# Kernel tuning notes

Measured on AMD Instinct MI355X. Metric: run time of the kernel, lower is better.

The kernel has to match this reference:

```python
import jax, jax.numpy as jnp
import numpy as np

N = 50000      # nodes
E = 800000     # edges (before self loops)
IN = 128       # in_channels
HID = 128      # 2*out_channels
OUT = 64       # out_channels
NEG_SLOPE = 0.2


def _gat_conv(x, src, dst, W, a_src, a_dst, b, n_nodes):
    """Single-head PyG GATConv (concat=True, heads=1, self-loops already added)."""
    h = x @ W                                   # [N, F]
    alpha_s = h @ a_src                         # [N]
    alpha_d = h @ a_dst                         # [N]
    e = alpha_s[src] + alpha_d[dst]             # [E'] logits per edge j->i
    e = jnp.where(e > 0, e, NEG_SLOPE * e)      # LeakyReLU(0.2)
    # segment softmax over destination node
    m = jax.ops.segment_max(e, dst, num_segments=n_nodes)   # [N]
    w = jnp.exp(e - m[dst])                                   # [E']
    denom = jax.ops.segment_sum(w, dst, num_segments=n_nodes) # [N]
    alpha = w / denom[dst]                                     # [E']
    out = jax.ops.segment_sum(alpha[:, None] * h[src], dst, num_segments=n_nodes)
    return out + b


def _with_self_loops(edge_index, n_nodes):
    loop = jnp.arange(n_nodes, dtype=edge_index.dtype)
    src = jnp.concatenate([edge_index[0], loop])
    dst = jnp.concatenate([edge_index[1], loop])
    return src, dst


def setup_inputs() -> dict:
    key = jax.random.key(0)
    ks = jax.random.split(key, 10)
    s = 0.1
    return {
        "x": jax.random.normal(ks[0], (N, IN), jnp.float32),
        "edge_index": jax.random.randint(ks[1], (2, E), 0, N, jnp.int32),
        "W1": jax.random.normal(ks[2], (IN, HID), jnp.float32) * s,
        "a1_src": jax.random.normal(ks[3], (HID,), jnp.float32) * s,
        "a1_dst": jax.random.normal(ks[4], (HID,), jnp.float32) * s,
        "b1": jnp.zeros((HID,), jnp.float32),
        "W2": jax.random.normal(ks[5], (HID, OUT), jnp.float32) * s,
        "a2_src": jax.random.normal(ks[6], (OUT,), jnp.float32) * s,
        "a2_dst": jax.random.normal(ks[7], (OUT,), jnp.float32) * s,
        "b2": jnp.zeros((OUT,), jnp.float32),
    }


def reference(x, edge_index, W1, a1_src, a1_dst, b1, W2, a2_src, a2_dst, b2):
    src, dst = _with_self_loops(edge_index, N)
    h = _gat_conv(x, src, dst, W1, a1_src, a1_dst, b1, N)
    h = jax.nn.relu(h)
    return _gat_conv(h, src, dst, W2, a2_src, a2_dst, b2, N)
```

## Files before the change

kernel.cpp:

```cpp
#include <hip/hip_runtime.h>
#include <hip/hip_bf16.h>


#define BCAP 4096

typedef __attribute__((ext_vector_type(8))) short bf16x8;
typedef __attribute__((ext_vector_type(4))) float f32x4;

__device__ __forceinline__ unsigned short bf16bits(float f){
  __hip_bfloat16 b = __float2bfloat16(f);
  return *(unsigned short*)&b;
}
__device__ __forceinline__ float bf16lo(unsigned int v){ return __uint_as_float(v << 16); }
__device__ __forceinline__ float bf16hi(unsigned int v){ return __uint_as_float(v & 0xFFFF0000u); }

__global__ __launch_bounds__(256) void prep_w_both(
    const float* __restrict__ W1, const float* __restrict__ W2,
    const float* __restrict__ a2s, const float* __restrict__ a2d,
    unsigned short* __restrict__ W1t, unsigned short* __restrict__ W2t,
    float* __restrict__ vas, float* __restrict__ vad)
{
  int b = blockIdx.x, t = threadIdx.x;
  if (b < 48){
    int idx = b*256 + t;
    if (idx < 8192){
      int n = idx >> 6, k2 = idx & 63;
      float a = W1[(size_t)(2*k2)*128 + n];
      float c = W1[(size_t)(2*k2+1)*128 + n];
      ushort2 o; o.x = bf16bits(a); o.y = bf16bits(c);
      *(ushort2*)&W1t[(size_t)n*128 + 2*k2] = o;
    } else {
      int r = idx - 8192;
      int n = r >> 6, k2 = r & 63;
      float a = W2[(size_t)(2*k2)*64 + n];
      float c = W2[(size_t)(2*k2+1)*64 + n];
      ushort2 o; o.x = bf16bits(a); o.y = bf16bits(c);
      *(ushort2*)&W2t[(size_t)n*128 + 2*k2] = o;
    }
  } else {
    int k = t & 127;
    const float* av = (t < 128) ? a2s : a2d;
    float* ov = (t < 128) ? vas : vad;
    float s = 0.f;
    for (int n=0; n<64; n++) s += W2[(size_t)k*64 + n] * av[n];
    ov[k] = s;
  }
}

template<int NC, bool FUSE>
__device__ __forceinline__ void gemm_body(
    const float* __restrict__ Af, const unsigned short* __restrict__ Ah,
    const unsigned short* __restrict__ Wt,
    const float* __restrict__ avs, const float* __restrict__ avd,
    unsigned short* __restrict__ H, float* __restrict__ as_, float* __restrict__ ad_,
    int M, int rowBase, unsigned short* As, unsigned short* Ws)
{
  const int K = 128;
  int t = threadIdx.x;
  if (Af){
    #pragma unroll
    for (int i=0;i<8;i++){
      int idx = t + i*256; int r = idx>>5, k4 = idx&31;
      int grow = rowBase + r;
      float4 v = (grow<M) ? *(const float4*)&Af[(size_t)grow*K + k4*4]
                          : make_float4(0.f,0.f,0.f,0.f);
      ushort4 o; o.x=bf16bits(v.x); o.y=bf16bits(v.y); o.z=bf16bits(v.z); o.w=bf16bits(v.w);
      *(ushort4*)&As[r*136 + k4*4] = o;
    }
  } else {
    #pragma unroll
    for (int i=0;i<4;i++){
      int idx = t + i*256; int r = idx>>4, k8 = idx&15;
      int grow = rowBase + r;
      uint4 v = (grow<M) ? *(const uint4*)&Ah[(size_t)grow*K + k8*8]
                         : make_uint4(0u,0u,0u,0u);
      *(uint4*)&As[r*136 + k8*8] = v;
    }
  }
  #pragma unroll
  for (int i=0;i<NC/16;i++){
    int idx = t + i*256; int n = idx>>4, k8 = idx&15;
    *(uint4*)&Ws[n*136 + k8*8] = *(const uint4*)&Wt[(size_t)n*K + k8*8];
  }
  __syncthreads();

  int wave = t>>6, lane = t&63, ln = lane&15, q = lane>>4;
  f32x4 acc[NC/16];
  #pragma unroll
  for (int nt=0; nt<NC/16; nt++) acc[nt] = (f32x4){0.f,0.f,0.f,0.f};
  #pragma unroll
  for (int kk=0;kk<4;kk++){
    bf16x8 a = *(const bf16x8*)&As[(wave*16+ln)*136 + kk*32 + q*8];
    #pragma unroll
    for (int nt=0; nt<NC/16; nt++){
      bf16x8 b = *(const bf16x8*)&Ws[(nt*16+ln)*136 + kk*32 + q*8];
      acc[nt] = __builtin_amdgcn_mfma_f32_16x16x32_bf16(a, b, acc[nt], 0, 0, 0);
    }
  }
  float asl[NC/16], adl[NC/16];
  if (FUSE){
    #pragma unroll
    for (int nt=0; nt<NC/16; nt++){ asl[nt]=avs[nt*16+ln]; adl[nt]=avd[nt*16+ln]; }
  }
  #pragma unroll
  for (int i=0;i<4;i++){
    int grow = rowBase + wave*16 + q*4 + i;
    if (grow < M){
      float ps=0.f, pd=0.f;
      #pragma unroll
      for (int nt=0; nt<NC/16; nt++){
        float v = acc[nt][i];
        H[(size_t)grow*NC + nt*16 + ln] = bf16bits(v);
        if (FUSE){ ps += v*asl[nt]; pd += v*adl[nt]; }
      }
      if (FUSE){
        #pragma unroll
        for (int d=1; d<16; d<<=1){ ps += __shfl_xor(ps,d); pd += __shfl_xor(pd,d); }
        if (ln==0){ atomicAdd(&as_[grow], ps); atomicAdd(&ad_[grow], pd); }
      }
    }
  }
}

__global__ __launch_bounds__(256) void scatter_or_gemm(
    const int* __restrict__ src, const int* __restrict__ dst,
    int* __restrict__ bucketCount, unsigned int* __restrict__ gbuf, int E, int B,
    const float* __restrict__ x, const unsigned short* __restrict__ W1t,
    const float* __restrict__ a1s, const float* __restrict__ a1d,
    unsigned short* __restrict__ h1, float* __restrict__ as1, float* __restrict__ ad1,
    int M)
{
  __shared__ unsigned short smem[64*136 + 128*136];
  int t = threadIdx.x;
  if ((int)blockIdx.x >= B){
    gemm_body<128, true>(x, nullptr, W1t, a1s, a1d, h1, as1, ad1, M,
                         (blockIdx.x - B)*64, smem, smem + 64*136);
    return;
  }
  int* hist = (int*)smem;
  int* base = hist + 512;
  int e0 = blockIdx.x * 2048;
  hist[t] = 0; hist[t+256] = 0;
  __syncthreads();
  int sv[8], dv[8];
  #pragma unroll
  for (int k=0;k<8;k++){
    int i = e0 + t + k*256;
    if (i < E){ sv[k]=src[i]; dv[k]=dst[i]; atomicAdd(&hist[dv[k]>>7], 1); }
    else { sv[k] = -1; dv[k] = 0; }
  }
  __syncthreads();
  int h0 = hist[t], h1c = hist[t+256];
  if (h0 > 0)  base[t]     = atomicAdd(&bucketCount[t],     h0);
  if (h1c > 0) base[t+256] = atomicAdd(&bucketCount[t+256], h1c);
  __syncthreads();
  hist[t] = 0; hist[t+256] = 0;
  __syncthreads();
  #pragma unroll
  for (int k=0;k<8;k++){
    if (sv[k] >= 0){
      int b = dv[k] >> 7;
      int r = base[b] + atomicAdd(&hist[b], 1);
      if (r < BCAP)
        gbuf[(size_t)b*BCAP + r] = ((unsigned)(dv[k] & 127) << 16) | (unsigned)sv[k];
    }
  }
}

__global__ __launch_bounds__(256) void fine_sort(
    const unsigned int* __restrict__ gbuf, const int* __restrict__ bucketCount,
    int* __restrict__ offs, int* __restrict__ srcS, int N, int E, int B)
{
  __shared__ int sh[512];
  __shared__ int h[128];
  __shared__ int pre[128];
  __shared__ int rank[128];
  int b = blockIdx.x, t = threadIdx.x;
  {
    int i0 = t, i1 = t + 256;
    int nd0 = 0, nd1 = 0;
    if (i0 < B){ int lo=i0*128; nd0 = (N-lo<128)?(N-lo):128; }
    if (i1 < B){ int lo=i1*128; nd1 = (N-lo<128)?(N-lo):128; }
    sh[i0] = (i0 < B ? bucketCount[i0] : 0) + nd0;
    sh[i1] = (i1 < B ? bucketCount[i1] : 0) + nd1;
    __syncthreads();
    for (int d=1; d<512; d<<=1){
      int x0 = (i0 >= d) ? sh[i0-d] : 0;
      int x1 = (i1 >= d) ? sh[i1-d] : 0;
      __syncthreads();
      sh[i0] += x0; sh[i1] += x1;
      __syncthreads();
    }
  }
  int cnt = bucketCount[b]; if (cnt > BCAP) cnt = BCAP;
  int lo = b*128;
  int nd = (N - lo < 128) ? (N - lo) : 128;
  int base = sh[b] - (cnt + nd);
  if (b == 0 && t == 0) offs[N] = E + N;
  if (t < 128){ h[t] = 0; rank[t] = 0; }
  __syncthreads();
  for (int i = t; i < cnt; i += 256)
    atomicAdd(&h[(gbuf[(size_t)b*BCAP + i] >> 16) & 127], 1);
  __syncthreads();
  if (t < 128) pre[t] = (t < nd) ? (h[t] + 1) : 0;
  __syncthreads();
  for (int d=1; d<128; d<<=1){
    int x = (t >= d && t < 128) ? pre[t-d] : 0;
    __syncthreads();
    if (t < 128) pre[t] += x;
    __syncthreads();
  }
  int seg = (t < nd) ? (h[t] + 1) : 0;
  int ex  = (t < 128) ? (pre[t] - seg) : 0;
  if (t < nd){
    offs[lo + t] = base + ex;
    srcS[base + ex] = lo + t;
  }
  __syncthreads();
  if (t < 128) pre[t] = ex;
  __syncthreads();
  for (int i = t; i < cnt; i += 256){
    unsigned e = gbuf[(size_t)b*BCAP + i];
    int dl = (e >> 16) & 127;
    int s  = e & 0xFFFF;
    int r  = atomicAdd(&rank[dl], 1);
    srcS[base + pre[dl] + 1 + r] = s;
  }
}

__global__ __launch_bounds__(256) void edge_agg128(
    const int* __restrict__ offs, const int* __restrict__ srcS,
    const float* __restrict__ asrc, const float* __restrict__ adst,
    const unsigned short* __restrict__ Hin, const float* __restrict__ bias,
    unsigned short* __restrict__ outp,
    const float* __restrict__ vas, const float* __restrict__ vad,
    float* __restrict__ as2, float* __restrict__ ad2, int n)
{
  int wid  = (blockIdx.x * 256 + threadIdx.x) >> 6;
  int lane = threadIdx.x & 63;
  if (wid >= n) return;
  int beg = offs[wid], end = offs[wid+1];
  float ad = adst[wid];
  int qw = lane >> 4, ql = lane & 15;
  float acc[8] = {}; float denom = 0.f;
  for (int base = beg; base < end; base += 64){
    int m = end - base; if (m > 64) m = 64;
    int   sv = (lane < m) ? srcS[base + lane] : 0;
    float av = (lane < m) ? asrc[sv] : 0.f;
    float ev = av + ad;
    ev = (ev > 0.f) ? ev : 0.2f*ev;
    float wv = (lane < m) ? __expf(ev) : 0.f;
    for (int j = 0; j < m; j += 4){
      int idx = j + qw;
      int   s = __shfl(sv, idx);
      float w = __shfl(wv, idx);
      uint4 hv = *(const uint4*)&Hin[(size_t)s*128 + ql*8];
      denom += w;
      acc[0]+=w*bf16lo(hv.x); acc[1]+=w*bf16hi(hv.x);
      acc[2]+=w*bf16lo(hv.y); acc[3]+=w*bf16hi(hv.y);
      acc[4]+=w*bf16lo(hv.z); acc[5]+=w*bf16hi(hv.z);
      acc[6]+=w*bf16lo(hv.w); acc[7]+=w*bf16hi(hv.w);
    }
  }
  denom += __shfl_xor(denom,16); denom += __shfl_xor(denom,32);
  #pragma unroll
  for (int k=0;k<8;k++){ acc[k]+=__shfl_xor(acc[k],16); acc[k]+=__shfl_xor(acc[k],32); }
  if (qw == 0){
    float inv = 1.0f / denom;
    float ps = 0.f, pd = 0.f;
    unsigned short o[8];
    #pragma unroll
    for (int k=0;k<8;k++){
      float v = fmaxf(acc[k]*inv + bias[ql*8+k], 0.f);
      o[k] = bf16bits(v);
      ps += v * vas[ql*8+k];
      pd += v * vad[ql*8+k];
    }
    *(uint4*)&outp[(size_t)wid*128 + ql*8] = *(uint4*)o;
    #pragma unroll
    for (int d=1; d<16; d<<=1){ ps += __shfl_xor(ps,d); pd += __shfl_xor(pd,d); }
    if (ql == 0){ as2[wid] = ps; ad2[wid] = pd; }
  }
}

__global__ __launch_bounds__(256) void gemm2_k(
    const unsigned short* __restrict__ A, const unsigned short* __restrict__ Wt,
    unsigned short* __restrict__ H, int M)
{
  __shared__ unsigned short smem[64*136 + 64*136];
  gemm_body<64, false>(nullptr, A, Wt, nullptr, nullptr, H, nullptr, nullptr,
                       M, blockIdx.x*64, smem, smem + 64*136);
}

__global__ __launch_bounds__(256) void edge_agg64(
    const int* __restrict__ offs, const int* __restrict__ srcS,
    const float* __restrict__ asrc, const float* __restrict__ adst,
    const unsigned short* __restrict__ Hin, const float* __restrict__ bias,
    float* __restrict__ outp, int n)
{
  int wid  = (blockIdx.x * 256 + threadIdx.x) >> 6;
  int lane = threadIdx.x & 63;
  if (wid >= n) return;
  int beg = offs[wid], end = offs[wid+1];
  float ad = adst[wid];
  int ew = lane >> 3, el = lane & 7;
  float acc[8] = {}; float denom = 0.f;
  for (int base = beg; base < end; base += 64){
    int m = end - base; if (m > 64) m = 64;
    int   sv = (lane < m) ? srcS[base + lane] : 0;
    float av = (lane < m) ? asrc[sv] : 0.f;
    float ev = av + ad;
    ev = (ev > 0.f) ? ev : 0.2f*ev;
    float wv = (lane < m) ? __expf(ev) : 0.f;
    for (int j = 0; j < m; j += 8){
      int idx = j + ew;
      int   s = __shfl(sv, idx);
      float w = __shfl(wv, idx);
      uint4 hv = *(const uint4*)&Hin[(size_t)s*64 + el*8];
      denom += w;
      acc[0]+=w*bf16lo(hv.x); acc[1]+=w*bf16hi(hv.x);
      acc[2]+=w*bf16lo(hv.y); acc[3]+=w*bf16hi(hv.y);
      acc[4]+=w*bf16lo(hv.z); acc[5]+=w*bf16hi(hv.z);
      acc[6]+=w*bf16lo(hv.w); acc[7]+=w*bf16hi(hv.w);
    }
  }
  denom += __shfl_xor(denom,8); denom += __shfl_xor(denom,16); denom += __shfl_xor(denom,32);
  #pragma unroll
  for (int k=0;k<8;k++){
    acc[k]+=__shfl_xor(acc[k],8); acc[k]+=__shfl_xor(acc[k],16); acc[k]+=__shfl_xor(acc[k],32);
  }
  if (ew == 0){
    float inv = 1.0f / denom;
    float4 o0, o1;
    o0.x = acc[0]*inv + bias[el*8+0]; o0.y = acc[1]*inv + bias[el*8+1];
    o0.z = acc[2]*inv + bias[el*8+2]; o0.w = acc[3]*inv + bias[el*8+3];
    o1.x = acc[4]*inv + bias[el*8+4]; o1.y = acc[5]*inv + bias[el*8+5];
    o1.z = acc[6]*inv + bias[el*8+6]; o1.w = acc[7]*inv + bias[el*8+7];
    *(float4*)&outp[(size_t)wid*64 + el*8]     = o0;
    *(float4*)&outp[(size_t)wid*64 + el*8 + 4] = o1;
  }
}

extern "C" void kernel_launch(void* const* d_in, const int* in_sizes, int n_in,
                              void* d_out, int out_size, void* d_ws, size_t ws_size,
                              hipStream_t stream) {
  const int IN = 128, HID = 128, OUT = 64;
  const int N = in_sizes[0] / IN;
  const int E = in_sizes[1] / 2;
  const int B = (N + 127) / 128;

  const float* x    = (const float*)d_in[0];
  const int*   ei   = (const int*)d_in[1];
  const float* W1   = (const float*)d_in[2];
  const float* a1s  = (const float*)d_in[3];
  const float* a1d  = (const float*)d_in[4];
  const float* b1   = (const float*)d_in[5];
  const float* W2   = (const float*)d_in[6];
  const float* a2s  = (const float*)d_in[7];
  const float* a2d  = (const float*)d_in[8];
  const float* b2   = (const float*)d_in[9];
  float* out = (float*)d_out;

  char* w = (char*)d_ws;
  unsigned short* W1t = (unsigned short*)w; w += (size_t)HID*IN*2;
  unsigned short* W2t = (unsigned short*)w; w += (size_t)OUT*HID*2;
  unsigned short* h1    = (unsigned short*)w; w += (size_t)N*128*2;
  unsigned short* hrelu = (unsigned short*)w; w += (size_t)N*128*2;
  unsigned short* h2 = h1;
  float* as1   = (float*)w; w += (size_t)N*4;
  float* ad1   = (float*)w; w += (size_t)N*4;
  float* as2   = (float*)w; w += (size_t)N*4;
  float* ad2   = (float*)w; w += (size_t)N*4;
  float* vas   = (float*)w; w += 128*4;
  float* vad   = (float*)w; w += 128*4;
  int* offs    = (int*)w;   w += (size_t)(N+1)*4;
  int* bucketCount = (int*)w; w += 512*4;
  int* srcS    = (int*)w;   w += (size_t)(E+N)*4;
  unsigned int* gbuf = (unsigned int*)w; w += (size_t)B*BCAP*4;

  const int* esrc = ei;
  const int* edst = ei + E;

  hipMemsetAsync(bucketCount, 0, 512*4, stream);
  hipMemsetAsync(as1, 0, (size_t)2*N*4, stream);
  hipLaunchKernelGGL(prep_w_both, dim3(49), dim3(256), 0, stream,
                     W1, W2, a2s, a2d, W1t, W2t, vas, vad);
  hipLaunchKernelGGL(scatter_or_gemm, dim3(B + (N+63)/64), dim3(256), 0, stream,
                     esrc, edst, bucketCount, gbuf, E, B,
                     x, W1t, a1s, a1d, h1, as1, ad1, N);
  hipLaunchKernelGGL(fine_sort, dim3(B), dim3(256), 0, stream,
                     gbuf, bucketCount, offs, srcS, N, E, B);
  hipLaunchKernelGGL(edge_agg128, dim3((N*64+255)/256), dim3(256), 0, stream,
                     offs, srcS, as1, ad1, h1, b1, hrelu, vas, vad, as2, ad2, N);
  hipLaunchKernelGGL(gemm2_k, dim3((N+63)/64), dim3(256), 0, stream,
                     hrelu, W2t, h2, N);
  hipLaunchKernelGGL(edge_agg64, dim3((N*64+255)/256), dim3(256), 0, stream,
                     offs, srcS, as2, ad2, h2, b2, out, N);
}
```

Measured before the change: 210.9 us.

## Fold memsets into prep kernel, chunk W staging, widen fine_sort, unroll gathers

Replaces the two hipMemsetAsync calls with extra blocks in the prep kernel that zero bucketCount and the attention-score buffers, removing two launches. The layer-1 GEMM now stages W in two 64-column chunks, halving its shared memory so more blocks can be resident, at the cost of an extra barrier pair. fine_sort runs with 512 threads per block and a simpler one-element-per-thread scan. Both edge aggregation loops now process two neighbours per iteration so that more gather loads are in flight.

```diff
diff --git a/kernel.cpp b/kernel.cpp
--- a/kernel.cpp
+++ b/kernel.cpp
@@ -14,11 +14,12 @@
 __device__ __forceinline__ float bf16lo(unsigned int v){ return __uint_as_float(v << 16); }
 __device__ __forceinline__ float bf16hi(unsigned int v){ return __uint_as_float(v & 0xFFFF0000u); }
 
-__global__ __launch_bounds__(256) void prep_w_both(
+__global__ __launch_bounds__(256) void prep_all(
     const float* __restrict__ W1, const float* __restrict__ W2,
     const float* __restrict__ a2s, const float* __restrict__ a2d,
     unsigned short* __restrict__ W1t, unsigned short* __restrict__ W2t,
-    float* __restrict__ vas, float* __restrict__ vad)
+    float* __restrict__ vas, float* __restrict__ vad,
+    float* __restrict__ zeroBase, int nZero4, int* __restrict__ bucketCount)
 {
   int b = blockIdx.x, t = threadIdx.x;
   if (b < 48){
@@ -37,13 +38,19 @@
       ushort2 o; o.x = bf16bits(a); o.y = bf16bits(c);
       *(ushort2*)&W2t[(size_t)n*128 + 2*k2] = o;
     }
-  } else {
+  } else if (b == 48){
     int k = t & 127;
     const float* av = (t < 128) ? a2s : a2d;
     float* ov = (t < 128) ? vas : vad;
     float s = 0.f;
     for (int n=0; n<64; n++) s += W2[(size_t)k*64 + n] * av[n];
     ov[k] = s;
+  } else if (b == 49){
+    bucketCount[t] = 0; bucketCount[t+256] = 0;
+  } else {
+    int idx4 = (b-50)*256 + t;
+    if (idx4 < nZero4)
+      ((float4*)zeroBase)[idx4] = make_float4(0.f,0.f,0.f,0.f);
   }
 }
 
@@ -77,24 +84,28 @@
       *(uint4*)&As[r*136 + k8*8] = v;
     }
   }
-  #pragma unroll
-  for (int i=0;i<NC/16;i++){
-    int idx = t + i*256; int n = idx>>4, k8 = idx&15;
-    *(uint4*)&Ws[n*136 + k8*8] = *(const uint4*)&Wt[(size_t)n*K + k8*8];
-  }
-  __syncthreads();
-
   int wave = t>>6, lane = t&63, ln = lane&15, q = lane>>4;
   f32x4 acc[NC/16];
   #pragma unroll
   for (int nt=0; nt<NC/16; nt++) acc[nt] = (f32x4){0.f,0.f,0.f,0.f};
-  #pragma unroll
-  for (int kk=0;kk<4;kk++){
-    bf16x8 a = *(const bf16x8*)&As[(wave*16+ln)*136 + kk*32 + q*8];
-    #pragma unroll
-    for (int nt=0; nt<NC/16; nt++){
-      bf16x8 b = *(const bf16x8*)&Ws[(nt*16+ln)*136 + kk*32 + q*8];
-      acc[nt] = __builtin_amdgcn_mfma_f32_16x16x32_bf16(a, b, acc[nt], 0, 0, 0);
+
+  #pragma unroll
+  for (int ch=0; ch<NC/64; ++ch){
+    __syncthreads();
+    #pragma unroll
+    for (int i=0;i<4;i++){
+      int idx = t + i*256; int n = idx>>4, k8 = idx&15;
+      *(uint4*)&Ws[n*136 + k8*8] = *(const uint4*)&Wt[(size_t)(ch*64+n)*K + k8*8];
+    }
+    __syncthreads();
+    #pragma unroll
+    for (int kk=0;kk<4;kk++){
+      bf16x8 a = *(const bf16x8*)&As[(wave*16+ln)*136 + kk*32 + q*8];
+      #pragma unroll
+      for (int nt=0; nt<4; nt++){
+        bf16x8 b = *(const bf16x8*)&Ws[(nt*16+ln)*136 + kk*32 + q*8];
+        acc[ch*4+nt] = __builtin_amdgcn_mfma_f32_16x16x32_bf16(a, b, acc[ch*4+nt], 0, 0, 0);
+      }
     }
   }
   float asl[NC/16], adl[NC/16];
@@ -130,7 +141,7 @@
     unsigned short* __restrict__ h1, float* __restrict__ as1, float* __restrict__ ad1,
     int M)
 {
-  __shared__ unsigned short smem[64*136 + 128*136];
+  __shared__ unsigned short smem[64*136 + 64*136];
   int t = threadIdx.x;
   if ((int)blockIdx.x >= B){
     gemm_body<128, true>(x, nullptr, W1t, a1s, a1d, h1, as1, ad1, M,
@@ -167,7 +178,7 @@
   }
 }
 
-__global__ __launch_bounds__(256) void fine_sort(
+__global__ __launch_bounds__(512) void fine_sort(
     const unsigned int* __restrict__ gbuf, const int* __restrict__ bucketCount,
     int* __restrict__ offs, int* __restrict__ srcS, int N, int E, int B)
 {
@@ -177,18 +188,14 @@
   __shared__ int rank[128];
   int b = blockIdx.x, t = threadIdx.x;
   {
-    int i0 = t, i1 = t + 256;
-    int nd0 = 0, nd1 = 0;
-    if (i0 < B){ int lo=i0*128; nd0 = (N-lo<128)?(N-lo):128; }
-    if (i1 < B){ int lo=i1*128; nd1 = (N-lo<128)?(N-lo):128; }
-    sh[i0] = (i0 < B ? bucketCount[i0] : 0) + nd0;
-    sh[i1] = (i1 < B ? bucketCount[i1] : 0) + nd1;
+    int nd_t = 0;
+    if (t < B){ int lo=t*128; nd_t = (N-lo<128)?(N-lo):128; }
+    sh[t] = (t < B ? bucketCount[t] : 0) + nd_t;
     __syncthreads();
     for (int d=1; d<512; d<<=1){
-      int x0 = (i0 >= d) ? sh[i0-d] : 0;
-      int x1 = (i1 >= d) ? sh[i1-d] : 0;
+      int x = (t >= d) ? sh[t-d] : 0;
       __syncthreads();
-      sh[i0] += x0; sh[i1] += x1;
+      sh[t] += x;
       __syncthreads();
     }
   }
@@ -199,7 +206,7 @@
   if (b == 0 && t == 0) offs[N] = E + N;
   if (t < 128){ h[t] = 0; rank[t] = 0; }
   __syncthreads();
-  for (int i = t; i < cnt; i += 256)
+  for (int i = t; i < cnt; i += 512)
     atomicAdd(&h[(gbuf[(size_t)b*BCAP + i] >> 16) & 127], 1);
   __syncthreads();
   if (t < 128) pre[t] = (t < nd) ? (h[t] + 1) : 0;
@@ -219,7 +226,7 @@
   __syncthreads();
   if (t < 128) pre[t] = ex;
   __syncthreads();
-  for (int i = t; i < cnt; i += 256){
+  for (int i = t; i < cnt; i += 512){
     unsigned e = gbuf[(size_t)b*BCAP + i];
     int dl = (e >> 16) & 127;
     int s  = e & 0xFFFF;
@@ -250,16 +257,17 @@
     float ev = av + ad;
     ev = (ev > 0.f) ? ev : 0.2f*ev;
     float wv = (lane < m) ? __expf(ev) : 0.f;
-    for (int j = 0; j < m; j += 4){
-      int idx = j + qw;
-      int   s = __shfl(sv, idx);
-      float w = __shfl(wv, idx);
-      uint4 hv = *(const uint4*)&Hin[(size_t)s*128 + ql*8];
-      denom += w;
-      acc[0]+=w*bf16lo(hv.x); acc[1]+=w*bf16hi(hv.x);
-      acc[2]+=w*bf16lo(hv.y); acc[3]+=w*bf16hi(hv.y);
-      acc[4]+=w*bf16lo(hv.z); acc[5]+=w*bf16hi(hv.z);
-      acc[6]+=w*bf16lo(hv.w); acc[7]+=w*bf16hi(hv.w);
+    for (int j = 0; j < m; j += 8){
+      int i0 = j + qw, i1 = j + 4 + qw;
+      int   s0 = __shfl(sv, i0), s1 = __shfl(sv, i1);
+      float w0 = __shfl(wv, i0), w1 = __shfl(wv, i1);
+      uint4 ha = *(const uint4*)&Hin[(size_t)s0*128 + ql*8];
+      uint4 hb = *(const uint4*)&Hin[(size_t)s1*128 + ql*8];
+      denom += w0 + w1;
+      acc[0]+=w0*bf16lo(ha.x)+w1*bf16lo(hb.x); acc[1]+=w0*bf16hi(ha.x)+w1*bf16hi(hb.x);
+      acc[2]+=w0*bf16lo(ha.y)+w1*bf16lo(hb.y); acc[3]+=w0*bf16hi(ha.y)+w1*bf16hi(hb.y);
+      acc[4]+=w0*bf16lo(ha.z)+w1*bf16lo(hb.z); acc[5]+=w0*bf16hi(ha.z)+w1*bf16hi(hb.z);
+      acc[6]+=w0*bf16lo(ha.w)+w1*bf16lo(hb.w); acc[7]+=w0*bf16hi(ha.w)+w1*bf16hi(hb.w);
     }
   }
   denom += __shfl_xor(denom,16); denom += __shfl_xor(denom,32);
@@ -312,16 +320,17 @@
     float ev = av + ad;
     ev = (ev > 0.f) ? ev : 0.2f*ev;
     float wv = (lane < m) ? __expf(ev) : 0.f;
-    for (int j = 0; j < m; j += 8){
-      int idx = j + ew;
-      int   s = __shfl(sv, idx);
-      float w = __shfl(wv, idx);
-      uint4 hv = *(const uint4*)&Hin[(size_t)s*64 + el*8];
-      denom += w;
-      acc[0]+=w*bf16lo(hv.x); acc[1]+=w*bf16hi(hv.x);
-      acc[2]+=w*bf16lo(hv.y); acc[3]+=w*bf16hi(hv.y);
-      acc[4]+=w*bf16lo(hv.z); acc[5]+=w*bf16hi(hv.z);
-      acc[6]+=w*bf16lo(hv.w); acc[7]+=w*bf16hi(hv.w);
+    for (int j = 0; j < m; j += 16){
+      int i0 = j + ew, i1 = j + 8 + ew;
+      int   s0 = __shfl(sv, i0), s1 = __shfl(sv, i1);
+      float w0 = __shfl(wv, i0), w1 = __shfl(wv, i1);
+      uint4 ha = *(const uint4*)&Hin[(size_t)s0*64 + el*8];
+      uint4 hb = *(const uint4*)&Hin[(size_t)s1*64 + el*8];
+      denom += w0 + w1;
+      acc[0]+=w0*bf16lo(ha.x)+w1*bf16lo(hb.x); acc[1]+=w0*bf16hi(ha.x)+w1*bf16hi(hb.x);
+      acc[2]+=w0*bf16lo(ha.y)+w1*bf16lo(hb.y); acc[3]+=w0*bf16hi(ha.y)+w1*bf16hi(hb.y);
+      acc[4]+=w0*bf16lo(ha.z)+w1*bf16lo(hb.z); acc[5]+=w0*bf16hi(ha.z)+w1*bf16hi(hb.z);
+      acc[6]+=w0*bf16lo(ha.w)+w1*bf16lo(hb.w); acc[7]+=w0*bf16hi(ha.w)+w1*bf16hi(hb.w);
     }
   }
   denom += __shfl_xor(denom,8); denom += __shfl_xor(denom,16); denom += __shfl_xor(denom,32);
@@ -380,15 +389,15 @@
 
   const int* esrc = ei;
   const int* edst = ei + E;
-
-  hipMemsetAsync(bucketCount, 0, 512*4, stream);
-  hipMemsetAsync(as1, 0, (size_t)2*N*4, stream);
-  hipLaunchKernelGGL(prep_w_both, dim3(49), dim3(256), 0, stream,
-                     W1, W2, a2s, a2d, W1t, W2t, vas, vad);
+  int nZero4 = (2*N) / 4;
+  int zeroBlocks = (nZero4 + 255) / 256;
+
+  hipLaunchKernelGGL(prep_all, dim3(50 + zeroBlocks), dim3(256), 0, stream,
+                     W1, W2, a2s, a2d, W1t, W2t, vas, vad, as1, nZero4, bucketCount);
   hipLaunchKernelGGL(scatter_or_gemm, dim3(B + (N+63)/64), dim3(256), 0, stream,
                      esrc, edst, bucketCount, gbuf, E, B,
                      x, W1t, a1s, a1d, h1, as1, ad1, N);
-  hipLaunchKernelGGL(fine_sort, dim3(B), dim3(256), 0, stream,
+  hipLaunchKernelGGL(fine_sort, dim3(B), dim3(512), 0, stream,
                      gbuf, bucketCount, offs, srcS, N, E, B);
   hipLaunchKernelGGL(edge_agg128, dim3((N*64+255)/256), dim3(256), 0, stream,
                      offs, srcS, as1, ad1, h1, b1, hrelu, vas, vad, as2, ad2, N);
```

Result: faster. 195.1 us (-7.5%).
